# Kernel optimization log

Hardware: AMD Instinct MI355X
Metric: run time of the kernel (lower is better)

## Reference

```python
import jax, jax.numpy as jnp
import numpy as np

B, N, DIM, H, DH = 8, 1024, 768, 12, 64
INNER = H * DH
SCALE = DH ** -0.5


def _bias_idx(n):
    # Reproduce the offset->id mapping from the torch __init__ loop:
    # offsets are first seen in row-major (p1, p2) order, so
    # id(0)=0, id(-k)=k (k=1..n-1), id(+k)=n-1+k.
    i = np.arange(n)[:, None]
    j = np.arange(n)[None, :]
    off = i - j
    idx = np.where(off <= 0, -off, n - 1 + off)
    return jnp.asarray(idx, dtype=jnp.int32)  # (n, n), values in [0, 2n-2]


def setup_inputs() -> dict:
    key = jax.random.key(0)
    ks = jax.random.split(key, 5)
    x = jax.random.normal(ks[0], (B, N, DIM), dtype=jnp.float32)
    w_qkv = jax.random.normal(ks[1], (DIM, 3 * INNER), dtype=jnp.float32) * (DIM ** -0.5)
    bias_table = jax.random.normal(ks[2], (H, 2 * N - 1), dtype=jnp.float32) * 0.02
    w_out = jax.random.normal(ks[3], (INNER, DIM), dtype=jnp.float32) * (INNER ** -0.5)
    b_out = jnp.zeros((DIM,), dtype=jnp.float32)
    bias_idx = _bias_idx(N)
    return {"x": x, "w_qkv": w_qkv, "bias_table": bias_table,
            "w_out": w_out, "b_out": b_out, "bias_idx": bias_idx}


def reference(x, w_qkv, bias_table, w_out, b_out, bias_idx):
    b, n, _ = x.shape
    qkv = x @ w_qkv  # (b, n, 3*inner)
    q, k, v = jnp.split(qkv, 3, axis=-1)
    def heads(t):
        return t.reshape(b, n, H, DH).transpose(0, 2, 1, 3)  # (b, h, n, d)
    q, k, v = heads(q), heads(k), heads(v)
    bias = bias_table[:, bias_idx]  # (h, n, n), gathered per-head relpos bias
    dots = jnp.einsum('bhid,bhjd->bhij', q, k) * SCALE + bias[None]
    attn = jax.nn.softmax(dots, axis=-1)
    out = jnp.einsum('bhij,bhjd->bhid', attn, v)
    out = out.transpose(0, 2, 1, 3).reshape(b, n, INNER)
    return out @ w_out + b_out
```

## Files before the change

### kernel.cpp

```cpp
#include <hip/hip_runtime.h>
#include <hip/hip_bf16.h>
#include <stdint.h>

typedef unsigned short u16;
typedef unsigned int u32;
typedef __bf16 bf16x8 __attribute__((ext_vector_type(8)));
typedef _Float16 f16x8 __attribute__((ext_vector_type(8)));
typedef float f32x4 __attribute__((ext_vector_type(4)));
typedef float f32x16 __attribute__((ext_vector_type(16)));
typedef unsigned short u16x4 __attribute__((ext_vector_type(4)));
typedef unsigned int u32x4 __attribute__((ext_vector_type(4)));

#define SEQ     1024
#define DIM     768
#define NH      12
#define QKV_LD  2304
#define LOG2E   1.4426950408889634f
#define C1      0.18033688f

__device__ __forceinline__ float bf2f(u16 u) {
    union { unsigned v; float f; } x; x.v = ((unsigned)u) << 16; return x.f;
}
__device__ __forceinline__ u16 f2bf(float f) {
    union { float f; unsigned v; } x; x.f = f;
    unsigned r = (x.v + 0x7FFFu + ((x.v >> 16) & 1u)) >> 16;
    return (u16)r;
}
__device__ __forceinline__ void store_out(u16* p, float v)  { *p = f2bf(v); }
__device__ __forceinline__ void store_out(float* p, float v){ *p = v; }

__device__ __forceinline__ void async16(void* lds, const void* g) {
    __builtin_amdgcn_global_load_lds(
        (const __attribute__((address_space(1))) unsigned*)(uintptr_t)g,
        (__attribute__((address_space(3))) unsigned*)(unsigned)(uintptr_t)lds,
        16, 0, 0);
}

__global__ __launch_bounds__(256) void cvt_k(const float* __restrict__ in,
                                             u16* __restrict__ out) {
    int i = (blockIdx.x * 256 + threadIdx.x) * 4;
    float4 v = *(const float4*)(in + i);
    u16x4 o = { f2bf(v.x), f2bf(v.y), f2bf(v.z), f2bf(v.w) };
    *(u16x4*)(out + i) = o;
}

__global__ __launch_bounds__(256) void transpose_k(const float* __restrict__ in,
                                                   u16* __restrict__ out,
                                                   int R, int C) {
    __shared__ __align__(16) float t[32][33];
    int c0 = blockIdx.x * 32, r0 = blockIdx.y * 32;
    int tx = threadIdx.x & 31, ty = threadIdx.x >> 5;
#pragma unroll
    for (int i = 0; i < 32; i += 8)
        t[ty + i][tx] = in[(size_t)(r0 + ty + i) * C + c0 + tx];
    __syncthreads();
#pragma unroll
    for (int i = 0; i < 32; i += 8)
        out[(size_t)(c0 + ty + i) * R + r0 + tx] = f2bf(t[tx][ty + i]);
}

__global__ __launch_bounds__(256) void vt_k(const u16* __restrict__ qkv,
                                            _Float16* __restrict__ vT) {
    __shared__ __align__(16) u16 t[32][33];
    int bh = blockIdx.z;
    int b = bh / 12, h = bh % 12;
    int key0 = blockIdx.x * 32, dh0 = blockIdx.y * 32;
    int tx = threadIdx.x & 31, ty = threadIdx.x >> 5;
#pragma unroll
    for (int i = 0; i < 32; i += 8)
        t[ty + i][tx] = qkv[(size_t)(b * SEQ + key0 + ty + i) * QKV_LD +
                            1536 + h * 64 + dh0 + tx];
    __syncthreads();
#pragma unroll
    for (int i = 0; i < 32; i += 8)
        vT[(size_t)(bh * 64 + dh0 + ty + i) * SEQ + key0 + tx] =
            (_Float16)bf2f(t[tx][ty + i]);
}

template <int HAS_BIAS, typename OUT_T>
__global__ __launch_bounds__(256) void gemm_bt(const u16* __restrict__ A,
                                               const u16* __restrict__ Bt,
                                               const float* __restrict__ bias,
                                               OUT_T* __restrict__ C,
                                               int M, int N, int K) {
    __shared__ __align__(16) u16 sA[128 * 64];
    __shared__ __align__(16) u16 sB[128 * 64];
    const int tid = threadIdx.x;
    const int lane = tid & 63;
    const int quad = lane >> 4, l16 = lane & 15;
    const int wave = tid >> 6;

    const int nwg = gridDim.x * gridDim.y;
    const int wgid = blockIdx.y * gridDim.x + blockIdx.x;
    const int swz = (wgid & 7) * (nwg >> 3) + (wgid >> 3);
    const int m0 = (swz % gridDim.x) * 128, n0 = (swz / gridDim.x) * 128;
    const int wm = (wave >> 1) * 64, wn = (wave & 1) * 64;

    const int co0 = (quad ^ (l16 & 7)) * 8;
    f32x4 acc[4][4] = {};

    for (int k0 = 0; k0 < K; k0 += 64) {
        __syncthreads();
#pragma unroll
        for (int rep = 0; rep < 4; ++rep) {
            int i = rep * 256 + tid;
            int row = i >> 3;
            int c = (i & 7) ^ (row & 7);
            async16(&sA[i * 8], A + (size_t)(m0 + row) * K + k0 + c * 8);
            async16(&sB[i * 8], Bt + (size_t)(n0 + row) * K + k0 + c * 8);
        }
        __syncthreads();

#pragma unroll
        for (int ks = 0; ks < 2; ++ks) {
            const int co = co0 ^ (ks * 32);
            bf16x8 af[4], bfr[4];
#pragma unroll
            for (int mi = 0; mi < 4; ++mi)
                af[mi] = *(const bf16x8*)&sA[(wm + mi * 16 + l16) * 64 + co];
#pragma unroll
            for (int nj = 0; nj < 4; ++nj)
                bfr[nj] = *(const bf16x8*)&sB[(wn + nj * 16 + l16) * 64 + co];
#pragma unroll
            for (int mi = 0; mi < 4; ++mi)
#pragma unroll
                for (int nj = 0; nj < 4; ++nj)
                    acc[mi][nj] = __builtin_amdgcn_mfma_f32_16x16x32_bf16(
                        af[mi], bfr[nj], acc[mi][nj], 0, 0, 0);
        }
    }

#pragma unroll
    for (int mi = 0; mi < 4; ++mi) {
#pragma unroll
        for (int nj = 0; nj < 4; ++nj) {
            int col = n0 + wn + nj * 16 + l16;
            float bv = HAS_BIAS ? bias[col] : 0.0f;
#pragma unroll
            for (int r = 0; r < 4; ++r) {
                int row = m0 + wm + mi * 16 + quad * 4 + r;
                store_out(&C[(size_t)row * N + col], acc[mi][nj][r] + bv);
            }
        }
    }
}

__global__ __launch_bounds__(256, 3) void attn_k(const u16* __restrict__ qkv,
                                                 const _Float16* __restrict__ vT,
                                                 const float* __restrict__ bias_table,
                                                 u16* __restrict__ out) {
    __shared__ __align__(16) u16 sK[2][64 * 64];
    __shared__ __align__(16) _Float16 sV[2][64 * 64];
    __shared__ __align__(16) float sLut[2048];

    const int tid = threadIdx.x;
    const int wave = tid >> 6, lane = tid & 63;
    const int l31 = lane & 31, hi = lane >> 5;
    const int bh = blockIdx.x;
    const int b = bh / NH, h = bh % NH;
    const int q0 = blockIdx.y * 128, wq = wave * 32;

    for (int i = tid; i < 2047; i += 256)
        sLut[i] = LOG2E * bias_table[h * 2047 + (i <= 1023 ? 1023 - i : i)];

    bf16x8 qf[4];
#pragma unroll
    for (int ks = 0; ks < 4; ++ks)
        qf[ks] = *(const bf16x8*)(qkv +
            (size_t)(b * SEQ + q0 + wq + l31) * QKV_LD + h * 64 + ks * 16 + hi * 8);

    const u16* kgp[2];
    const _Float16* vgp[2];
    int lds_i[2];
#pragma unroll
    for (int rep = 0; rep < 2; ++rep) {
        int i = rep * 256 + wave * 64 + lane;
        int row = i >> 3;
        int c = (i & 7) ^ (row & 7);
        kgp[rep] = qkv + (size_t)(b * SEQ + row) * QKV_LD + 768 + h * 64 + c * 8;
        vgp[rep] = vT + (size_t)(bh * 64 + row) * SEQ + c * 8;
        lds_i[rep] = i * 8;
    }

    const int ib0 = 1023 + q0 + wq + l31;
    const int hi4 = hi * 4;
    const int l7 = l31 & 7;

#pragma unroll
    for (int rep = 0; rep < 2; ++rep) {
        async16(&sK[0][lds_i[rep]], kgp[rep]);
        async16(&sV[0][lds_i[rep]], vgp[rep]);
        kgp[rep] += (size_t)64 * QKV_LD;
        vgp[rep] += 64;
    }
    __syncthreads();

    f32x16 o[2] = {};
    f32x16 osum = {};
    const u32x4 onebits = { 0x3C003C00u, 0x3C003C00u, 0x3C003C00u, 0x3C003C00u };
    const f16x8 ones = __builtin_bit_cast(f16x8, onebits);

    for (int kt = 0; kt < SEQ / 64; ++kt) {
        const int cur = kt & 1;
        if (kt + 1 < SEQ / 64) {
            const int nxt = cur ^ 1;
#pragma unroll
            for (int rep = 0; rep < 2; ++rep) {
                async16(&sK[nxt][lds_i[rep]], kgp[rep]);
                async16(&sV[nxt][lds_i[rep]], vgp[rep]);
                kgp[rep] += (size_t)64 * QKV_LD;
                vgp[rep] += 64;
            }
        }
        const u16* sKc = sK[cur];
        const _Float16* sVc = sV[cur];

        f16x8 pfrag[4];
#pragma unroll
        for (int t = 0; t < 2; ++t) {
            const u16* kr = sKc + (t * 32 + l31) * 64;
            f32x16 s = {};
#pragma unroll
            for (int ks = 0; ks < 4; ++ks) {
                int slot = (2 * ks + hi) ^ l7;
                bf16x8 af = *(const bf16x8*)(kr + slot * 8);
                s = __builtin_amdgcn_mfma_f32_32x32x16_bf16(af, qf[ks], s, 0, 0, 0);
            }
            const int ibt = ib0 - kt * 64 - t * 32 - hi4;
            u32 wlo[4], whi[4];
#pragma unroll
            for (int g = 0; g < 4; ++g) {
                const float* bw = &sLut[ibt - 8 * g];
                float p0 = __builtin_amdgcn_exp2f(s[4 * g + 0] * C1 + bw[0]);
                float p1 = __builtin_amdgcn_exp2f(s[4 * g + 1] * C1 + bw[-1]);
                float p2 = __builtin_amdgcn_exp2f(s[4 * g + 2] * C1 + bw[-2]);
                float p3 = __builtin_amdgcn_exp2f(s[4 * g + 3] * C1 + bw[-3]);
                wlo[g] = __builtin_bit_cast(u32, __builtin_amdgcn_cvt_pkrtz(p0, p1));
                whi[g] = __builtin_bit_cast(u32, __builtin_amdgcn_cvt_pkrtz(p2, p3));
            }
#pragma unroll
            for (int c = 0; c < 2; ++c) {
                auto rlo = __builtin_amdgcn_permlane32_swap(
                    wlo[2 * c], wlo[2 * c + 1], false, false);
                auto rhi = __builtin_amdgcn_permlane32_swap(
                    whi[2 * c], whi[2 * c + 1], false, false);
                u32x4 f = { rlo[0], rhi[0], rlo[1], rhi[1] };
                pfrag[t * 2 + c] = __builtin_bit_cast(f16x8, f);
            }
        }

#pragma unroll
        for (int kg = 0; kg < 4; ++kg)
            osum = __builtin_amdgcn_mfma_f32_32x32x16_f16(ones, pfrag[kg], osum, 0, 0, 0);
#pragma unroll
        for (int dt = 0; dt < 2; ++dt) {
            const _Float16* vr = sVc + (dt * 32 + l31) * 64;
#pragma unroll
            for (int kg = 0; kg < 4; ++kg) {
                int slot = (2 * kg + hi) ^ l7;
                f16x8 vf = *(const f16x8*)(vr + slot * 8);
                o[dt] = __builtin_amdgcn_mfma_f32_32x32x16_f16(vf, pfrag[kg], o[dt], 0, 0, 0);
            }
        }

        if (kt + 1 < SEQ / 64) {
            asm volatile("s_waitcnt vmcnt(4)" ::: "memory");
            __builtin_amdgcn_s_barrier();
        }
    }

    float inv = __builtin_amdgcn_rcpf(osum[0]);
    size_t rowbase = (size_t)(b * SEQ + q0 + wq + l31) * DIM + h * 64 + hi4;
#pragma unroll
    for (int dt = 0; dt < 2; ++dt) {
#pragma unroll
        for (int g = 0; g < 4; ++g) {
            u16x4 pk = { f2bf(o[dt][4 * g + 0] * inv), f2bf(o[dt][4 * g + 1] * inv),
                         f2bf(o[dt][4 * g + 2] * inv), f2bf(o[dt][4 * g + 3] * inv) };
            *(u16x4*)&out[rowbase + dt * 32 + 8 * g] = pk;
        }
    }
}

extern "C" void kernel_launch(void* const* d_in, const int* in_sizes, int n_in,
                              void* d_out, int out_size, void* d_ws, size_t ws_size,
                              hipStream_t stream) {
    const float* x          = (const float*)d_in[0];
    const float* w_qkv      = (const float*)d_in[1];
    const float* bias_table = (const float*)d_in[2];
    const float* w_out      = (const float*)d_in[3];
    const float* b_out      = (const float*)d_in[4];
    float* out = (float*)d_out;

    char* ws = (char*)d_ws;
    u16* ws_qkv        = (u16*)(ws);
    u16* ws_attn       = (u16*)(ws + 37748736);
    u16* ws_xb         = (u16*)(ws + 50331648);
    u16* ws_wqkvT      = (u16*)(ws + 62914560);
    u16* ws_woutT      = (u16*)(ws + 66453504);
    _Float16* ws_vT    = (_Float16*)(ws + 67633152);

    cvt_k<<<8 * 1024 * 768 / 1024, 256, 0, stream>>>(x, ws_xb);
    transpose_k<<<dim3(2304 / 32, 768 / 32), 256, 0, stream>>>(w_qkv, ws_wqkvT, 768, 2304);
    transpose_k<<<dim3(768 / 32, 768 / 32), 256, 0, stream>>>(w_out, ws_woutT, 768, 768);

    gemm_bt<0, u16><<<dim3(8192 / 128, 2304 / 128), 256, 0, stream>>>(
        ws_xb, ws_wqkvT, nullptr, ws_qkv, 8192, 2304, 768);

    vt_k<<<dim3(SEQ / 32, 2, 8 * NH), 256, 0, stream>>>(ws_qkv, ws_vT);

    attn_k<<<dim3(8 * NH, SEQ / 128, 1), 256, 0, stream>>>(ws_qkv, ws_vT, bias_table, ws_attn);

    gemm_bt<1, float><<<dim3(8192 / 128, 768 / 128), 256, 0, stream>>>(
        ws_attn, ws_woutT, b_out, out, 8192, 768, 768);
}
```

Measured before the change: 201.6 us.

## Triple-buffer K/V loads in attention, shrink bias LUT, add MFMA priority and XCD GEMM remap

The attention kernel moves from double to triple buffering of K/V tiles, prefetching two tiles ahead to hide global load latency. The wait counts are adjusted at the tail. The relative-position LUT is trimmed to the 1151 entries this query block needs, offsetting the extra LDS used by the third buffer. s_setprio raises wave priority around the PV MFMAs. The GEMM tile mapping is changed so each XCD gets a contiguous band of M tiles, aiming for better L2 reuse. The extra LDS may limit occupancy.

```diff
diff --git a/kernel.cpp b/kernel.cpp
--- a/kernel.cpp
+++ b/kernel.cpp
@@ -90,10 +90,11 @@
     const int quad = lane >> 4, l16 = lane & 15;
     const int wave = tid >> 6;
 
-    const int nwg = gridDim.x * gridDim.y;
     const int wgid = blockIdx.y * gridDim.x + blockIdx.x;
-    const int swz = (wgid & 7) * (nwg >> 3) + (wgid >> 3);
-    const int m0 = (swz % gridDim.x) * 128, n0 = (swz / gridDim.x) * 128;
+    const int xcd = wgid & 7, idx = wgid >> 3;
+    const int CM = gridDim.x >> 3;
+    const int m0 = (xcd * CM + idx % CM) * 128;
+    const int n0 = (idx / CM) * 128;
     const int wm = (wave >> 1) * 64, wn = (wave & 1) * 64;
 
     const int co0 = (quad ^ (l16 & 7)) * 8;
@@ -149,9 +150,9 @@
                                                  const _Float16* __restrict__ vT,
                                                  const float* __restrict__ bias_table,
                                                  u16* __restrict__ out) {
-    __shared__ __align__(16) u16 sK[2][64 * 64];
-    __shared__ __align__(16) _Float16 sV[2][64 * 64];
-    __shared__ __align__(16) float sLut[2048];
+    __shared__ __align__(16) u16 sK[3][64 * 64];
+    __shared__ __align__(16) _Float16 sV[3][64 * 64];
+    __shared__ __align__(16) float sLut[1152];
 
     const int tid = threadIdx.x;
     const int wave = tid >> 6, lane = tid & 63;
@@ -160,8 +161,10 @@
     const int b = bh / NH, h = bh % NH;
     const int q0 = blockIdx.y * 128, wq = wave * 32;
 
-    for (int i = tid; i < 2047; i += 256)
-        sLut[i] = LOG2E * bias_table[h * 2047 + (i <= 1023 ? 1023 - i : i)];
+    for (int i = tid; i < 1151; i += 256) {
+        int z = q0 + i;
+        sLut[i] = LOG2E * bias_table[h * 2047 + (z <= 1023 ? 1023 - z : z)];
+    }
 
     bf16x8 qf[4];
 #pragma unroll
@@ -182,32 +185,35 @@
         lds_i[rep] = i * 8;
     }
 
-    const int ib0 = 1023 + q0 + wq + l31;
+    const int ibW = 1023 + wq + l31;
     const int hi4 = hi * 4;
     const int l7 = l31 & 7;
 
 #pragma unroll
-    for (int rep = 0; rep < 2; ++rep) {
-        async16(&sK[0][lds_i[rep]], kgp[rep]);
-        async16(&sV[0][lds_i[rep]], vgp[rep]);
-        kgp[rep] += (size_t)64 * QKV_LD;
-        vgp[rep] += 64;
-    }
-    __syncthreads();
+    for (int bf = 0; bf < 2; ++bf)
+#pragma unroll
+        for (int rep = 0; rep < 2; ++rep) {
+            async16(&sK[bf][lds_i[rep]], kgp[rep]);
+            async16(&sV[bf][lds_i[rep]], vgp[rep]);
+            kgp[rep] += (size_t)64 * QKV_LD;
+            vgp[rep] += 64;
+        }
+    asm volatile("s_waitcnt vmcnt(4) lgkmcnt(0)" ::: "memory");
+    __builtin_amdgcn_s_barrier();
 
     f32x16 o[2] = {};
     f32x16 osum = {};
     const u32x4 onebits = { 0x3C003C00u, 0x3C003C00u, 0x3C003C00u, 0x3C003C00u };
     const f16x8 ones = __builtin_bit_cast(f16x8, onebits);
 
+    int cur = 0;
     for (int kt = 0; kt < SEQ / 64; ++kt) {
-        const int cur = kt & 1;
-        if (kt + 1 < SEQ / 64) {
-            const int nxt = cur ^ 1;
+        if (kt + 2 < SEQ / 64) {
+            int b2 = cur + 2; if (b2 >= 3) b2 -= 3;
 #pragma unroll
             for (int rep = 0; rep < 2; ++rep) {
-                async16(&sK[nxt][lds_i[rep]], kgp[rep]);
-                async16(&sV[nxt][lds_i[rep]], vgp[rep]);
+                async16(&sK[b2][lds_i[rep]], kgp[rep]);
+                async16(&sV[b2][lds_i[rep]], vgp[rep]);
                 kgp[rep] += (size_t)64 * QKV_LD;
                 vgp[rep] += 64;
             }
@@ -226,7 +232,7 @@
                 bf16x8 af = *(const bf16x8*)(kr + slot * 8);
                 s = __builtin_amdgcn_mfma_f32_32x32x16_bf16(af, qf[ks], s, 0, 0, 0);
             }
-            const int ibt = ib0 - kt * 64 - t * 32 - hi4;
+            const int ibt = ibW - kt * 64 - t * 32 - hi4;
             u32 wlo[4], whi[4];
 #pragma unroll
             for (int g = 0; g < 4; ++g) {
@@ -249,6 +255,7 @@
             }
         }
 
+        __builtin_amdgcn_s_setprio(1);
 #pragma unroll
         for (int kg = 0; kg < 4; ++kg)
             osum = __builtin_amdgcn_mfma_f32_32x32x16_f16(ones, pfrag[kg], osum, 0, 0, 0);
@@ -262,11 +269,16 @@
                 o[dt] = __builtin_amdgcn_mfma_f32_32x32x16_f16(vf, pfrag[kg], o[dt], 0, 0, 0);
             }
         }
-
-        if (kt + 1 < SEQ / 64) {
+        __builtin_amdgcn_s_setprio(0);
+
+        if (kt < 14) {
             asm volatile("s_waitcnt vmcnt(4)" ::: "memory");
             __builtin_amdgcn_s_barrier();
-        }
+        } else if (kt == 14) {
+            asm volatile("s_waitcnt vmcnt(0)" ::: "memory");
+            __builtin_amdgcn_s_barrier();
+        }
+        cur = (cur == 2) ? 0 : cur + 1;
     }
 
     float inv = __builtin_amdgcn_rcpf(osum[0]);
```

New measurement: 196.8 us. 1.02x faster.
